# Kernel tuning notes

Hardware: AMD Instinct MI355X
Metric: run time of the kernel (lower is better)

## Reference

```python
import jax, jax.numpy as jnp
import numpy as np
from jax import lax

N, DEG, D_IN, D_FEAT, D_HID, D_REP, G = 32768, 16, 128, 256, 256, 128, 64


def setup_inputs() -> dict:
    key = jax.random.key(0)
    ks = jax.random.split(key, 24)
    def w(k, shape):
        return (jax.random.normal(k, shape, jnp.float32) / np.sqrt(shape[0])).astype(jnp.float32)
    inp = {
        "in_feat": jax.random.normal(ks[0], (N, D_IN), jnp.float32),
        "neighbors": jax.random.randint(ks[1], (N, DEG), 0, N, jnp.int32),
        "node2graph": jnp.sort(jax.random.randint(ks[2], (N,), 0, G, jnp.int32)),
        # layer 1 (SAGEConv 128 -> 256, lstm aggregator: LSTM(128,128))
        "w_ih1": w(ks[3], (4 * D_IN, D_IN)),
        "w_hh1": w(ks[4], (4 * D_IN, D_IN)),
        "b_lstm1": jnp.zeros((4 * D_IN,), jnp.float32),
        "w_self1": w(ks[5], (D_IN, D_FEAT)),
        "w_neigh1": w(ks[6], (D_IN, D_FEAT)),
        "b1": jnp.zeros((D_FEAT,), jnp.float32),
        # layer 2 (SAGEConv 256 -> 256, LSTM(256,256))
        "w_ih2": w(ks[7], (4 * D_FEAT, D_FEAT)),
        "w_hh2": w(ks[8], (4 * D_FEAT, D_FEAT)),
        "b_lstm2": jnp.zeros((4 * D_FEAT,), jnp.float32),
        "w_self2": w(ks[9], (D_FEAT, D_HID)),
        "w_neigh2": w(ks[10], (D_FEAT, D_HID)),
        "b2": jnp.zeros((D_HID,), jnp.float32),
        # heads
        "w_mu": w(ks[11], (D_HID, D_REP)),
        "b_mu": jnp.zeros((D_REP,), jnp.float32),
        "w_sigma": w(ks[12], (D_HID, D_REP)),
        "b_sigma": jnp.zeros((D_REP,), jnp.float32),
    }
    return inp


def _lstm_agg(seq, w_ih, w_hh, b):
    # seq: [N, L, D] neighbor messages; LSTM with zero init, return final hidden h.
    n, _, d = seq.shape
    h0 = jnp.zeros((n, d), seq.dtype)
    def step(carry, x):
        h, c = carry
        gates = x @ w_ih.T + h @ w_hh.T + b  # [N, 4D]
        i, f, g, o = jnp.split(gates, 4, axis=-1)  # pytorch gate order i,f,g,o
        c = jax.nn.sigmoid(f) * c + jax.nn.sigmoid(i) * jnp.tanh(g)
        h = jax.nn.sigmoid(o) * jnp.tanh(c)
        return (h, c), None
    (h, _), _ = lax.scan(step, (h0, h0), jnp.swapaxes(seq, 0, 1))
    return h


def _sage_lstm(feat, neighbors, w_ih, w_hh, b_lstm, w_self, w_neigh, b):
    msgs = feat[neighbors]                      # irregular gather [N, DEG, D]
    h_n = _lstm_agg(msgs, w_ih, w_hh, b_lstm)   # [N, D]
    return feat @ w_self + h_n @ w_neigh + b


def reference(in_feat, neighbors, node2graph,
              w_ih1, w_hh1, b_lstm1, w_self1, w_neigh1, b1,
              w_ih2, w_hh2, b_lstm2, w_self2, w_neigh2, b2,
              w_mu, b_mu, w_sigma, b_sigma):
    h = _sage_lstm(in_feat, neighbors, w_ih1, w_hh1, b_lstm1, w_self1, w_neigh1, b1)
    h = jax.nn.relu(h)
    h = _sage_lstm(h, neighbors, w_ih2, w_hh2, b_lstm2, w_self2, w_neigh2, b2)
    # dgl.mean_nodes: per-graph mean over nodes
    sums = jax.ops.segment_sum(h, node2graph, num_segments=G)
    cnts = jax.ops.segment_sum(jnp.ones((h.shape[0],), h.dtype), node2graph, num_segments=G)
    x = sums / jnp.maximum(cnts, 1.0)[:, None]
    return (x @ w_mu + b_mu, x @ w_sigma + b_sigma)
```

## Files before the change

kernel.cpp:

```cpp
#include <hip/hip_runtime.h>
#include <hip/hip_bf16.h>
#include <cstddef>

#define NN_   32768
#define DEG_  16
#define D1_   128
#define D2_   256
#define G_    64
#define DREP_ 128

typedef __attribute__((ext_vector_type(8))) short bf16x8;
typedef __attribute__((ext_vector_type(4))) float f32x4;
typedef __attribute__((ext_vector_type(4))) unsigned short us4;
typedef unsigned short ushort_t;

__device__ __attribute__((aligned(16))) ushort_t g_feat1[(size_t)NN_ * D1_];
__device__ __attribute__((aligned(16))) ushort_t g_hfeat[(size_t)NN_ * D2_];
__device__ __attribute__((aligned(16))) ushort_t g_hA[(size_t)NN_ * D2_];
__device__ __attribute__((aligned(16))) ushort_t g_hB[(size_t)NN_ * D2_];
__device__ __attribute__((aligned(16))) ushort_t g_c[(size_t)NN_ * D2_];
__device__ __attribute__((aligned(16))) ushort_t g_P[(size_t)NN_ * 1024];
__device__ __attribute__((aligned(16))) float    g_outh[(size_t)NN_ * D2_];
__device__ __attribute__((aligned(16))) ushort_t g_wih1[512 * 128];
__device__ __attribute__((aligned(16))) ushort_t g_whh1[512 * 128];
__device__ __attribute__((aligned(16))) ushort_t g_wself1[256 * 128];
__device__ __attribute__((aligned(16))) ushort_t g_wneigh1[256 * 128];
__device__ __attribute__((aligned(16))) ushort_t g_wih2[1024 * 256];
__device__ __attribute__((aligned(16))) ushort_t g_whh2[1024 * 256];
__device__ __attribute__((aligned(16))) ushort_t g_wself2[256 * 256];
__device__ __attribute__((aligned(16))) ushort_t g_wneigh2[256 * 256];
__device__ float g_gsum[G_ * D2_];
__device__ int   g_gcnt[G_];

__device__ __forceinline__ ushort_t f2bf(float f) {
    unsigned int u = __float_as_uint(f);
    u += 0x7fffu + ((u >> 16) & 1u);
    return (ushort_t)(u >> 16);
}
__device__ __forceinline__ float bf2f(ushort_t u) {
    return __uint_as_float(((unsigned int)u) << 16);
}
__device__ __forceinline__ float sigf(float x) { return 1.f / (1.f + __expf(-x)); }
__device__ __forceinline__ float tanhf_(float x) { return 1.f - 2.f / (__expf(2.f * x) + 1.f); }

__global__ __launch_bounds__(256) void cvt_bf16(const float* __restrict__ src,
                                                ushort_t* __restrict__ dst, int n)
{
    int i = blockIdx.x * 256 + threadIdx.x;
    if (i < n) dst[i] = f2bf(src[i]);
}

__global__ __launch_bounds__(256) void cvt_bf16_T(const float* __restrict__ src,
                                                  ushort_t* __restrict__ dst, int K, int N)
{
    int i = blockIdx.x * 256 + threadIdx.x;
    if (i < K * N) {
        int k = i / N, n = i % N;
        dst[n * K + k] = f2bf(src[i]);
    }
}

template<bool DUAL, bool HAS_BIAS, bool RELU, bool OUTBF>
__global__ __launch_bounds__(256) void gemm_mfma(
    const ushort_t* __restrict__ A1, const ushort_t* __restrict__ B1,
    const ushort_t* __restrict__ A2, const ushort_t* __restrict__ B2,
    const float* __restrict__ bias, float* __restrict__ Cf,
    ushort_t* __restrict__ Cb, int M, int N, int K)
{
    __shared__ ushort_t As[64][72];
    __shared__ ushort_t Bs[64][72];
    const int tid = threadIdx.x;
    const int l = tid & 63, w = tid >> 6;
    const int m0 = blockIdx.y * 64, n0 = blockIdx.x * 64;

    f32x4 acc[4];
#pragma unroll
    for (int m = 0; m < 4; ++m) acc[m] = (f32x4){0.f, 0.f, 0.f, 0.f};

    const int npass = DUAL ? 2 : 1;
    for (int pass = 0; pass < npass; ++pass) {
        const ushort_t* __restrict__ A = (DUAL && pass) ? A2 : A1;
        const ushort_t* __restrict__ B = (DUAL && pass) ? B2 : B1;
        for (int k0 = 0; k0 < K; k0 += 64) {
#pragma unroll
            for (int i = 0; i < 2; ++i) {
                int cid = tid + 256 * i;
                int row = cid >> 3, col = (cid & 7) * 8;
                *(uint4*)&As[row][col] = *(const uint4*)&A[(size_t)(m0 + row) * K + k0 + col];
                *(uint4*)&Bs[row][col] = *(const uint4*)&B[(size_t)(n0 + row) * K + k0 + col];
            }
            __syncthreads();
#pragma unroll
            for (int kk = 0; kk < 64; kk += 32) {
                bf16x8 b = *(const bf16x8*)&Bs[16 * w + (l & 15)][kk + (l >> 4) * 8];
#pragma unroll
                for (int m = 0; m < 4; ++m) {
                    bf16x8 a = *(const bf16x8*)&As[16 * m + (l & 15)][kk + (l >> 4) * 8];
                    acc[m] = __builtin_amdgcn_mfma_f32_16x16x32_bf16(a, b, acc[m], 0, 0, 0);
                }
            }
            __syncthreads();
        }
    }

#pragma unroll
    for (int m = 0; m < 4; ++m) {
#pragma unroll
        for (int r = 0; r < 4; ++r) {
            int row = m0 + 16 * m + (l >> 4) * 4 + r;
            int col = n0 + 16 * w + (l & 15);
            float v = acc[m][r];
            if (HAS_BIAS) v += bias[col];
            if (RELU) v = fmaxf(v, 0.f);
            if (OUTBF) Cb[(size_t)row * N + col] = f2bf(v);
            else       Cf[(size_t)row * N + col] = v;
        }
    }
}

template<int D>
__global__ __launch_bounds__(256, 2) void lstm_step3(
    const ushort_t* __restrict__ h_prev, const ushort_t* __restrict__ whh,
    const ushort_t* __restrict__ P, const int* __restrict__ nbr,
    ushort_t* __restrict__ c, ushort_t* __restrict__ h_next, int t)
{
    constexpr int HP = D + 8;
    constexpr int KC = D / 32;
    constexpr int NT = 8;
    __shared__ ushort_t As[128][HP];

    const int tid = threadIdx.x;
    const int l = tid & 63, w = tid >> 6;
    const int lr = l & 15, lg = l >> 4;
    const int m0 = blockIdx.x * 128;
    const int d0 = blockIdx.y * 64;
    const int dd = d0 + w * 16 + lg * 4;

    int js[NT];
#pragma unroll
    for (int nt = 0; nt < NT; ++nt)
        js[nt] = nbr[(size_t)(m0 + nt * 16 + lr) * DEG_ + t];

    constexpr int CH = 128 * D / 8;
#pragma unroll
    for (int cid = tid; cid < CH; cid += 256) {
        int row = cid / (D / 8), cc = (cid % (D / 8)) * 8;
        *(uint4*)&As[row][cc] = *(const uint4*)&h_prev[(size_t)(m0 + row) * D + cc];
    }

    us4 pg[NT][4];
#pragma unroll
    for (int nt = 0; nt < NT; ++nt) {
        const size_t base = (size_t)js[nt] * (4 * D) + dd;
#pragma unroll
        for (int g = 0; g < 4; ++g)
            pg[nt][g] = *(const us4*)&P[base + g * D];
    }

    f32x4 acc[4][NT];
#pragma unroll
    for (int g = 0; g < 4; ++g)
#pragma unroll
        for (int nt = 0; nt < NT; ++nt) acc[g][nt] = (f32x4){0.f, 0.f, 0.f, 0.f};

    __syncthreads();

    const ushort_t* __restrict__ wbase = &whh[(size_t)(d0 + w * 16 + lr) * D + lg * 8];
#pragma unroll
    for (int kc = 0; kc < KC; ++kc) {
        bf16x8 a[4];
#pragma unroll
        for (int g = 0; g < 4; ++g)
            a[g] = *(const bf16x8*)&wbase[(size_t)g * D * D + kc * 32];
#pragma unroll
        for (int nt = 0; nt < NT; ++nt) {
            bf16x8 b = *(const bf16x8*)&As[nt * 16 + lr][kc * 32 + lg * 8];
#pragma unroll
            for (int g = 0; g < 4; ++g)
                acc[g][nt] = __builtin_amdgcn_mfma_f32_16x16x32_bf16(
                    a[g], b, acc[g][nt], 0, 0, 0);
        }
    }

#pragma unroll
    for (int nt = 0; nt < NT; ++nt) {
        const size_t ci = (size_t)(m0 + nt * 16 + lr) * D + dd;
        us4 cold = *(const us4*)&c[ci];
        us4 cnew, hnew;
#pragma unroll
        for (int r = 0; r < 4; ++r) {
            float gi = acc[0][nt][r] + bf2f(pg[nt][0][r]);
            float gf = acc[1][nt][r] + bf2f(pg[nt][1][r]);
            float gg = acc[2][nt][r] + bf2f(pg[nt][2][r]);
            float go = acc[3][nt][r] + bf2f(pg[nt][3][r]);
            float cn = sigf(gf) * bf2f(cold[r]) + sigf(gi) * tanhf_(gg);
            cnew[r] = f2bf(cn);
            hnew[r] = f2bf(sigf(go) * tanhf_(cn));
        }
        *(us4*)&c[ci] = cnew;
        *(us4*)&h_next[ci] = hnew;
    }
}

template<int D>
__global__ __launch_bounds__(256) void cell_first(
    const ushort_t* __restrict__ P, const int* __restrict__ nbr,
    ushort_t* __restrict__ c, ushort_t* __restrict__ h_out)
{
    int idx = blockIdx.x * 256 + threadIdx.x;
    int n = idx / D, d = idx % D;
    int j = nbr[n * DEG_];
    size_t base = (size_t)j * (4 * D);
    float gi = bf2f(P[base + d]);
    float gg = bf2f(P[base + 2 * D + d]);
    float go = bf2f(P[base + 3 * D + d]);
    float cn = sigf(gi) * tanhf_(gg);
    c[idx] = f2bf(cn);
    h_out[idx] = f2bf(sigf(go) * tanhf_(cn));
}

__global__ void graph_counts(const int* __restrict__ n2g, int* __restrict__ cnt)
{
    __shared__ int lb[G_ + 1];
    int g = threadIdx.x;
    if (g <= G_) {
        int lo = 0, hi = NN_;
        while (lo < hi) {
            int mid = (lo + hi) >> 1;
            if (n2g[mid] < g) lo = mid + 1; else hi = mid;
        }
        lb[g] = lo;
    }
    __syncthreads();
    if (g < G_) cnt[g] = lb[g + 1] - lb[g];
}

__global__ __launch_bounds__(256) void seg_sum(
    const float* __restrict__ X, const int* __restrict__ n2g,
    float* __restrict__ gsum)
{
    int d = threadIdx.x;
    int n_start = blockIdx.x * 64;
    int cur = n2g[n_start];
    float acc = 0.f;
    for (int n = n_start; n < n_start + 64; ++n) {
        int g = n2g[n];
        if (g != cur) {
            atomicAdd(&gsum[cur * D2_ + d], acc);
            acc = 0.f;
            cur = g;
        }
        acc += X[(size_t)n * D2_ + d];
    }
    atomicAdd(&gsum[cur * D2_ + d], acc);
}

__global__ __launch_bounds__(128) void head_kernel(
    const float* __restrict__ gsum, const int* __restrict__ cnt,
    const float* __restrict__ w_mu, const float* __restrict__ b_mu,
    const float* __restrict__ w_sig, const float* __restrict__ b_sig,
    float* __restrict__ out)
{
    __shared__ float x[D2_];
    int g = blockIdx.x, j = threadIdx.x;
    float inv = 1.f / fmaxf((float)cnt[g], 1.f);
    x[j] = gsum[g * D2_ + j] * inv;
    x[j + 128] = gsum[g * D2_ + 128 + j] * inv;
    __syncthreads();
    float mu = b_mu[j], sg = b_sig[j];
    for (int k = 0; k < D2_; ++k) {
        float xv = x[k];
        mu += xv * w_mu[k * DREP_ + j];
        sg += xv * w_sig[k * DREP_ + j];
    }
    out[g * DREP_ + j] = mu;
    out[G_ * DREP_ + g * DREP_ + j] = sg;
}

extern "C" void kernel_launch(void* const* d_in, const int* in_sizes, int n_in,
                              void* d_out, int out_size, void* d_ws, size_t ws_size,
                              hipStream_t stream)
{
    const float* in_feat   = (const float*)d_in[0];
    const int*   neighbors = (const int*)d_in[1];
    const int*   node2graph= (const int*)d_in[2];
    const float* w_ih1     = (const float*)d_in[3];
    const float* w_hh1     = (const float*)d_in[4];
    const float* b_lstm1   = (const float*)d_in[5];
    const float* w_self1   = (const float*)d_in[6];
    const float* w_neigh1  = (const float*)d_in[7];
    const float* b1        = (const float*)d_in[8];
    const float* w_ih2     = (const float*)d_in[9];
    const float* w_hh2     = (const float*)d_in[10];
    const float* b_lstm2   = (const float*)d_in[11];
    const float* w_self2   = (const float*)d_in[12];
    const float* w_neigh2  = (const float*)d_in[13];
    const float* b2        = (const float*)d_in[14];
    const float* w_mu      = (const float*)d_in[15];
    const float* b_mu      = (const float*)d_in[16];
    const float* w_sigma   = (const float*)d_in[17];
    const float* b_sigma   = (const float*)d_in[18];

    void *pF1, *pHF, *pHA, *pHB, *pC, *pP, *pOH;
    void *pWI1, *pWH1, *pWS1, *pWN1, *pWI2, *pWH2, *pWS2, *pWN2, *pGS, *pGC;
    hipGetSymbolAddress(&pF1, HIP_SYMBOL(g_feat1));
    hipGetSymbolAddress(&pHF, HIP_SYMBOL(g_hfeat));
    hipGetSymbolAddress(&pHA, HIP_SYMBOL(g_hA));
    hipGetSymbolAddress(&pHB, HIP_SYMBOL(g_hB));
    hipGetSymbolAddress(&pC,  HIP_SYMBOL(g_c));
    hipGetSymbolAddress(&pP,  HIP_SYMBOL(g_P));
    hipGetSymbolAddress(&pOH, HIP_SYMBOL(g_outh));
    hipGetSymbolAddress(&pWI1, HIP_SYMBOL(g_wih1));
    hipGetSymbolAddress(&pWH1, HIP_SYMBOL(g_whh1));
    hipGetSymbolAddress(&pWS1, HIP_SYMBOL(g_wself1));
    hipGetSymbolAddress(&pWN1, HIP_SYMBOL(g_wneigh1));
    hipGetSymbolAddress(&pWI2, HIP_SYMBOL(g_wih2));
    hipGetSymbolAddress(&pWH2, HIP_SYMBOL(g_whh2));
    hipGetSymbolAddress(&pWS2, HIP_SYMBOL(g_wself2));
    hipGetSymbolAddress(&pWN2, HIP_SYMBOL(g_wneigh2));
    hipGetSymbolAddress(&pGS, HIP_SYMBOL(g_gsum));
    hipGetSymbolAddress(&pGC, HIP_SYMBOL(g_gcnt));

    ushort_t* feat1 = (ushort_t*)pF1;
    ushort_t* hfeat = (ushort_t*)pHF;
    ushort_t* hA    = (ushort_t*)pHA;
    ushort_t* hB    = (ushort_t*)pHB;
    ushort_t* c     = (ushort_t*)pC;
    ushort_t* P     = (ushort_t*)pP;
    float*    outh  = (float*)pOH;
    ushort_t* wih1  = (ushort_t*)pWI1;
    ushort_t* whh1  = (ushort_t*)pWH1;
    ushort_t* wself1= (ushort_t*)pWS1;
    ushort_t* wneigh1=(ushort_t*)pWN1;
    ushort_t* wih2  = (ushort_t*)pWI2;
    ushort_t* whh2  = (ushort_t*)pWH2;
    ushort_t* wself2= (ushort_t*)pWS2;
    ushort_t* wneigh2=(ushort_t*)pWN2;
    float*    gsum  = (float*)pGS;
    int*      gcnt  = (int*)pGC;

    cvt_bf16<<<(NN_ * D1_ + 255) / 256, 256, 0, stream>>>(in_feat, feat1, NN_ * D1_);
    cvt_bf16<<<(512 * 128 + 255) / 256, 256, 0, stream>>>(w_ih1, wih1, 512 * 128);
    cvt_bf16<<<(512 * 128 + 255) / 256, 256, 0, stream>>>(w_hh1, whh1, 512 * 128);
    cvt_bf16_T<<<(128 * 256 + 255) / 256, 256, 0, stream>>>(w_self1, wself1, 128, 256);
    cvt_bf16_T<<<(128 * 256 + 255) / 256, 256, 0, stream>>>(w_neigh1, wneigh1, 128, 256);
    cvt_bf16<<<(1024 * 256 + 255) / 256, 256, 0, stream>>>(w_ih2, wih2, 1024 * 256);
    cvt_bf16<<<(1024 * 256 + 255) / 256, 256, 0, stream>>>(w_hh2, whh2, 1024 * 256);
    cvt_bf16_T<<<(256 * 256 + 255) / 256, 256, 0, stream>>>(w_self2, wself2, 256, 256);
    cvt_bf16_T<<<(256 * 256 + 255) / 256, 256, 0, stream>>>(w_neigh2, wneigh2, 256, 256);

    gemm_mfma<false, true, false, true>
        <<<dim3(512 / 64, NN_ / 64), 256, 0, stream>>>(
            feat1, wih1, nullptr, nullptr, b_lstm1, nullptr, P, NN_, 512, D1_);

    cell_first<D1_><<<(NN_ * D1_) / 256, 256, 0, stream>>>(P, neighbors, c, hA);
    for (int t = 1; t < DEG_; ++t) {
        const ushort_t* hp = (t & 1) ? hA : hB;
        ushort_t*       hn = (t & 1) ? hB : hA;
        lstm_step3<D1_><<<dim3(NN_ / 128, D1_ / 64), 256, 0, stream>>>(
            hp, whh1, P, neighbors, c, hn, t);
    }

    gemm_mfma<true, true, true, true>
        <<<dim3(256 / 64, NN_ / 64), 256, 0, stream>>>(
            feat1, wself1, hB, wneigh1, b1, nullptr, hfeat, NN_, D2_, D1_);

    gemm_mfma<false, true, false, true>
        <<<dim3(1024 / 64, NN_ / 64), 256, 0, stream>>>(
            hfeat, wih2, nullptr, nullptr, b_lstm2, nullptr, P, NN_, 1024, D2_);

    cell_first<D2_><<<(NN_ * D2_) / 256, 256, 0, stream>>>(P, neighbors, c, hA);
    for (int t = 1; t < DEG_; ++t) {
        const ushort_t* hp = (t & 1) ? hA : hB;
        ushort_t*       hn = (t & 1) ? hB : hA;
        lstm_step3<D2_><<<dim3(NN_ / 128, D2_ / 64), 256, 0, stream>>>(
            hp, whh2, P, neighbors, c, hn, t);
    }

    gemm_mfma<true, true, false, false>
        <<<dim3(256 / 64, NN_ / 64), 256, 0, stream>>>(
            hfeat, wself2, hB, wneigh2, b2, outh, nullptr, NN_, D2_, D2_);

    hipMemsetAsync(gsum, 0, (size_t)G_ * D2_ * sizeof(float), stream);
    graph_counts<<<1, 128, 0, stream>>>(node2graph, gcnt);
    seg_sum<<<NN_ / 64, 256, 0, stream>>>(outh, node2graph, gsum);
    head_kernel<<<G_, 128, 0, stream>>>(gsum, gcnt, w_mu, b_mu, w_sigma, b_sigma,
                                        (float*)d_out);
}
```

Baseline: 1.737 ms.

## Interleave LSTM gate projections and defer gathered loads to the epilogue

The input-projection GEMM now writes P in an interleaved layout so that the four gates (i,f,g,o) for 4 consecutive hidden units occupy 16 contiguous bf16 values. The per-step LSTM kernel then fetches them with two 16-byte loads per node instead of four scattered 8-byte loads, and cell_first indexes the same layout. The neighbor-index and P gather were moved from before the MFMA loop to the epilogue, which cuts register pressure but no longer overlaps those loads with the matmul. The GEMM epilogue stores become scattered for the PINT variant.

```diff
diff --git a/kernel.cpp b/kernel.cpp
--- a/kernel.cpp
+++ b/kernel.cpp
@@ -12,6 +12,7 @@
 typedef __attribute__((ext_vector_type(8))) short bf16x8;
 typedef __attribute__((ext_vector_type(4))) float f32x4;
 typedef __attribute__((ext_vector_type(4))) unsigned short us4;
+typedef __attribute__((ext_vector_type(8))) unsigned short us8;
 typedef unsigned short ushort_t;
 
 __device__ __attribute__((aligned(16))) ushort_t g_feat1[(size_t)NN_ * D1_];
@@ -60,7 +61,7 @@
     }
 }
 
-template<bool DUAL, bool HAS_BIAS, bool RELU, bool OUTBF>
+template<bool DUAL, bool HAS_BIAS, bool RELU, bool OUTBF, bool PINT>
 __global__ __launch_bounds__(256) void gemm_mfma(
     const ushort_t* __restrict__ A1, const ushort_t* __restrict__ B1,
     const ushort_t* __restrict__ A2, const ushort_t* __restrict__ B2,
@@ -112,8 +113,20 @@
             float v = acc[m][r];
             if (HAS_BIAS) v += bias[col];
             if (RELU) v = fmaxf(v, 0.f);
-            if (OUTBF) Cb[(size_t)row * N + col] = f2bf(v);
-            else       Cf[(size_t)row * N + col] = v;
+            if (OUTBF) {
+                size_t idx;
+                if (PINT) {
+                    int Dq = N >> 2;
+                    int g = col / Dq;
+                    int d = col - g * Dq;
+                    idx = (size_t)row * N + ((d >> 2) << 4) + (g << 2) + (d & 3);
+                } else {
+                    idx = (size_t)row * N + col;
+                }
+                Cb[idx] = f2bf(v);
+            } else {
+                Cf[(size_t)row * N + col] = v;
+            }
         }
     }
 }
@@ -136,11 +149,6 @@
     const int d0 = blockIdx.y * 64;
     const int dd = d0 + w * 16 + lg * 4;
 
-    int js[NT];
-#pragma unroll
-    for (int nt = 0; nt < NT; ++nt)
-        js[nt] = nbr[(size_t)(m0 + nt * 16 + lr) * DEG_ + t];
-
     constexpr int CH = 128 * D / 8;
 #pragma unroll
     for (int cid = tid; cid < CH; cid += 256) {
@@ -148,15 +156,6 @@
         *(uint4*)&As[row][cc] = *(const uint4*)&h_prev[(size_t)(m0 + row) * D + cc];
     }
 
-    us4 pg[NT][4];
-#pragma unroll
-    for (int nt = 0; nt < NT; ++nt) {
-        const size_t base = (size_t)js[nt] * (4 * D) + dd;
-#pragma unroll
-        for (int g = 0; g < 4; ++g)
-            pg[nt][g] = *(const us4*)&P[base + g * D];
-    }
-
     f32x4 acc[4][NT];
 #pragma unroll
     for (int g = 0; g < 4; ++g)
@@ -184,15 +183,21 @@
 
 #pragma unroll
     for (int nt = 0; nt < NT; ++nt) {
-        const size_t ci = (size_t)(m0 + nt * 16 + lr) * D + dd;
+        const int node = m0 + nt * 16 + lr;
+        const int j = nbr[(size_t)node * DEG_ + t];
+        const size_t pb = (size_t)j * (4 * D) + (((size_t)(dd >> 2)) << 4);
+        us8 p01 = *(const us8*)&P[pb];
+        us8 p23 = *(const us8*)&P[pb + 8];
+        const size_t ci = (size_t)node * D + dd;
         us4 cold = *(const us4*)&c[ci];
+
         us4 cnew, hnew;
 #pragma unroll
         for (int r = 0; r < 4; ++r) {
-            float gi = acc[0][nt][r] + bf2f(pg[nt][0][r]);
-            float gf = acc[1][nt][r] + bf2f(pg[nt][1][r]);
-            float gg = acc[2][nt][r] + bf2f(pg[nt][2][r]);
-            float go = acc[3][nt][r] + bf2f(pg[nt][3][r]);
+            float gi = acc[0][nt][r] + bf2f(p01[r]);
+            float gf = acc[1][nt][r] + bf2f(p01[4 + r]);
+            float gg = acc[2][nt][r] + bf2f(p23[r]);
+            float go = acc[3][nt][r] + bf2f(p23[4 + r]);
             float cn = sigf(gf) * bf2f(cold[r]) + sigf(gi) * tanhf_(gg);
             cnew[r] = f2bf(cn);
             hnew[r] = f2bf(sigf(go) * tanhf_(cn));
@@ -210,10 +215,10 @@
     int idx = blockIdx.x * 256 + threadIdx.x;
     int n = idx / D, d = idx % D;
     int j = nbr[n * DEG_];
-    size_t base = (size_t)j * (4 * D);
-    float gi = bf2f(P[base + d]);
-    float gg = bf2f(P[base + 2 * D + d]);
-    float go = bf2f(P[base + 3 * D + d]);
+    size_t base = (size_t)j * (4 * D) + (((size_t)(d >> 2)) << 4) + (d & 3);
+    float gi = bf2f(P[base]);
+    float gg = bf2f(P[base + 8]);
+    float go = bf2f(P[base + 12]);
     float cn = sigf(gi) * tanhf_(gg);
     c[idx] = f2bf(cn);
     h_out[idx] = f2bf(sigf(go) * tanhf_(cn));
@@ -349,7 +354,7 @@
     cvt_bf16_T<<<(256 * 256 + 255) / 256, 256, 0, stream>>>(w_self2, wself2, 256, 256);
     cvt_bf16_T<<<(256 * 256 + 255) / 256, 256, 0, stream>>>(w_neigh2, wneigh2, 256, 256);
 
-    gemm_mfma<false, true, false, true>
+    gemm_mfma<false, true, false, true, true>
         <<<dim3(512 / 64, NN_ / 64), 256, 0, stream>>>(
             feat1, wih1, nullptr, nullptr, b_lstm1, nullptr, P, NN_, 512, D1_);
 
@@ -361,11 +366,11 @@
             hp, whh1, P, neighbors, c, hn, t);
     }
 
-    gemm_mfma<true, true, true, true>
+    gemm_mfma<true, true, true, true, false>
         <<<dim3(256 / 64, NN_ / 64), 256, 0, stream>>>(
             feat1, wself1, hB, wneigh1, b1, nullptr, hfeat, NN_, D2_, D1_);
 
-    gemm_mfma<false, true, false, true>
+    gemm_mfma<false, true, false, true, true>
         <<<dim3(1024 / 64, NN_ / 64), 256, 0, stream>>>(
             hfeat, wih2, nullptr, nullptr, b_lstm2, nullptr, P, NN_, 1024, D2_);
 
@@ -377,7 +382,7 @@
             hp, whh2, P, neighbors, c, hn, t);
     }
 
-    gemm_mfma<true, true, false, false>
+    gemm_mfma<true, true, false, false, false>
         <<<dim3(256 / 64, NN_ / 64), 256, 0, stream>>>(
             hfeat, wself2, hB, wneigh2, b2, outh, nullptr, NN_, D2_, D2_);
 
```

After: 1.504 ms. 13.4% less time.
